# Kernel optimization log

Hardware: AMD Instinct MI355X
Metric: run time of the kernel (lower is better)

## Reference

```python
import jax, jax.numpy as jnp
import numpy as np

N, E, F_IN, H, C, G, OUT = 50000, 800000, 128, 4, 64, 64, 16
NEG_SLOPE = 0.2


def _gat_layer(x, src, dst, W, a_src, a_dst, b):
    # x: [N, Fin]; W: [Fin, H*C]; a_src/a_dst: [H, C]; b: [H*C]
    h = (x @ W).reshape(N, H, C)                      # [N,H,C]
    e_src = jnp.einsum('nhc,hc->nh', h, a_src)        # [N,H]
    e_dst = jnp.einsum('nhc,hc->nh', h, a_dst)
    e = jax.nn.leaky_relu(e_src[src] + e_dst[dst], NEG_SLOPE)  # [Etot,H]
    # segment softmax over edges sharing a destination node
    m = jax.ops.segment_max(e, dst, num_segments=N)   # [N,H]
    ex = jnp.exp(e - m[dst])
    s = jax.ops.segment_sum(ex, dst, num_segments=N)  # [N,H]
    alpha = ex / s[dst]                               # [Etot,H]
    msg = h[src] * alpha[:, :, None]                  # [Etot,H,C]
    out = jax.ops.segment_sum(msg, dst, num_segments=N)
    return out.reshape(N, H * C) + b


def setup_inputs() -> dict:
    key = jax.random.key(0)
    ks = jax.random.split(key, 12)
    x = jax.random.normal(ks[0], (N, F_IN), dtype=jnp.float32)
    edge_index = jax.random.randint(ks[1], (2, E), 0, N, dtype=jnp.int64)
    batch = jnp.sort(jax.random.randint(ks[2], (N,), 0, G, dtype=jnp.int64))
    hc = H * C
    W1 = jax.random.normal(ks[3], (F_IN, hc), dtype=jnp.float32) / np.sqrt(F_IN)
    a_src1 = jax.random.normal(ks[4], (H, C), dtype=jnp.float32) / np.sqrt(C)
    a_dst1 = jax.random.normal(ks[5], (H, C), dtype=jnp.float32) / np.sqrt(C)
    b1 = jnp.zeros((hc,), dtype=jnp.float32)
    W2 = jax.random.normal(ks[6], (hc, hc), dtype=jnp.float32) / np.sqrt(hc)
    a_src2 = jax.random.normal(ks[7], (H, C), dtype=jnp.float32) / np.sqrt(C)
    a_dst2 = jax.random.normal(ks[8], (H, C), dtype=jnp.float32) / np.sqrt(C)
    b2 = jnp.zeros((hc,), dtype=jnp.float32)
    Wlin = jax.random.normal(ks[9], (hc, OUT), dtype=jnp.float32) / np.sqrt(hc)
    blin = jnp.zeros((OUT,), dtype=jnp.float32)
    return dict(x=x, edge_index=edge_index, batch=batch,
                W1=W1, a_src1=a_src1, a_dst1=a_dst1, b1=b1,
                W2=W2, a_src2=a_src2, a_dst2=a_dst2, b2=b2,
                Wlin=Wlin, blin=blin)


def reference(x, edge_index, batch, W1, a_src1, a_dst1, b1,
              W2, a_src2, a_dst2, b2, Wlin, blin):
    # add self-loops (PyG GATConv default add_self_loops=True)
    loops = jnp.arange(N, dtype=edge_index.dtype)
    src = jnp.concatenate([edge_index[0], loops])
    dst = jnp.concatenate([edge_index[1], loops])
    h = jax.nn.relu(_gat_layer(x, src, dst, W1, a_src1, a_dst1, b1))
    h = jax.nn.relu(_gat_layer(h, src, dst, W2, a_src2, a_dst2, b2))
    # global mean pool over graphs
    sums = jax.ops.segment_sum(h, batch, num_segments=G)          # [G, H*C]
    cnt = jax.ops.segment_sum(jnp.ones((N,), h.dtype), batch, num_segments=G)
    pooled = sums / jnp.maximum(cnt, 1.0)[:, None]
    return pooled @ Wlin + blin                                    # [G, OUT]
```

## Files before the change

kernel.cpp:

```cpp
#include <hip/hip_runtime.h>
#include <hip/hip_fp16.h>

#define NN   50000
#define EE   800000
#define ETOT 850000
#define FIN  128
#define HC   256
#define NH   4
#define CH   64
#define NG   64
#define NOUT 16
#define NEG_SLOPE 0.2f

#define NBUCK 391
#define BCAP  4096
#define EPB   4096
#define NEB   208

typedef _Float16 f16x8 __attribute__((ext_vector_type(8)));
typedef float    f32x4 __attribute__((ext_vector_type(4)));

__global__ __launch_bounds__(256) void edge_bucket(const int* __restrict__ ei,
                                                   int* __restrict__ bucket_counts,
                                                   unsigned* __restrict__ buckets) {
    __shared__ int h[NBUCK];
    __shared__ int bb[NBUCK];
    const int tid = threadIdx.x;
    const int e0  = blockIdx.x * EPB;

    for (int t = tid; t < NBUCK; t += 256) h[t] = 0;
    __syncthreads();

    int srcs[16], dsts[16];
#pragma unroll
    for (int k = 0; k < 16; ++k) {
        int i = e0 + k * 256 + tid;
        int s = 0, d = -1;
        if (i < ETOT) {
            s = (i < EE) ? ei[i] : (i - EE);
            d = (i < EE) ? ei[EE + i] : (i - EE);
            atomicAdd(&h[d >> 7], 1);
        }
        srcs[k] = s; dsts[k] = d;
    }
    __syncthreads();

    for (int t = tid; t < NBUCK; t += 256) {
        bb[t] = atomicAdd(&bucket_counts[t], h[t]);
        h[t]  = 0;
    }
    __syncthreads();

#pragma unroll
    for (int k = 0; k < 16; ++k) {
        int d = dsts[k];
        if (d >= 0) {
            int b = d >> 7;
            int r = atomicAdd(&h[b], 1);
            int idx = bb[b] + r;
            if (idx < BCAP)
                buckets[(size_t)b * BCAP + idx] =
                    (unsigned)srcs[k] | ((unsigned)(d & 127) << 16);
        }
    }
}

__global__ __launch_bounds__(512) void bucket_scan(const int* __restrict__ counts,
                                                   int* __restrict__ basep,
                                                   int* __restrict__ rowptr) {
    __shared__ int lds[512];
    const int tid = threadIdx.x;
    int v = (tid < NBUCK) ? counts[tid] : 0;
    lds[tid] = v;
    __syncthreads();
    for (int off = 1; off < 512; off <<= 1) {
        int t = (tid >= off) ? lds[tid - off] : 0;
        __syncthreads();
        lds[tid] += t;
        __syncthreads();
    }
    if (tid < NBUCK) basep[tid] = lds[tid] - v;
    if (tid == 0) rowptr[NN] = ETOT;
}

__global__ __launch_bounds__(256) void bucket_to_csr(const unsigned* __restrict__ buckets,
                                                     const int* __restrict__ bucket_counts,
                                                     const int* __restrict__ bucket_base,
                                                     int* __restrict__ rowptr,
                                                     int* __restrict__ csr) {
    __shared__ int h[128], c[128], sc[128];
    const int b = blockIdx.x, tid = threadIdx.x;
    const int nb   = bucket_counts[b];
    const int base = bucket_base[b];

    if (tid < 128) h[tid] = 0;
    __syncthreads();
    for (int i = tid; i < nb; i += 256) {
        unsigned p = buckets[(size_t)b * BCAP + i];
        atomicAdd(&h[p >> 16], 1);
    }
    __syncthreads();
    if (tid < 128) sc[tid] = h[tid];
    __syncthreads();
    for (int off = 1; off < 128; off <<= 1) {
        int t = (tid < 128 && tid >= off) ? sc[tid - off] : 0;
        __syncthreads();
        if (tid < 128) sc[tid] += t;
        __syncthreads();
    }
    if (tid < 128) {
        int excl = sc[tid] - h[tid];
        c[tid] = excl;
        int node = (b << 7) + tid;
        if (node < NN) rowptr[node] = base + excl;
    }
    __syncthreads();
    for (int i = tid; i < nb; i += 256) {
        unsigned p = buckets[(size_t)b * BCAP + i];
        int pos = atomicAdd(&c[p >> 16], 1);
        csr[base + pos] = (int)(p & 0xFFFFu);
    }
}

__global__ void f32_to_f16_vec(const float* __restrict__ in, __half* __restrict__ out,
                               int n4) {
    int i = blockIdx.x * 256 + threadIdx.x;
    if (i >= n4) return;
    float4 v = *(const float4*)&in[(size_t)i * 4];
    __half h[4] = {__float2half(v.x), __float2half(v.y), __float2half(v.z), __float2half(v.w)};
    *(uint2*)&out[(size_t)i * 4] = *(uint2*)h;
}

__global__ void w_transpose_f16(const float* __restrict__ W, __half* __restrict__ Wt,
                                int K) {
    int idx = blockIdx.x * 256 + threadIdx.x;
    if (idx >= K * HC) return;
    int n = idx / K, k = idx - n * K;
    Wt[idx] = __float2half(W[(size_t)k * HC + n]);
}

__global__ __launch_bounds__(256) void gemm_f16(const __half* __restrict__ A16,
                                                const __half* __restrict__ Bt16,
                                                __half* __restrict__ C16,
                                                const float* __restrict__ a_src,
                                                const float* __restrict__ a_dst,
                                                float* __restrict__ es,
                                                float* __restrict__ ed,
                                                int M, int K) {
    __shared__ char lds[32768];
    const int tid  = threadIdx.x;
    const int m0   = blockIdx.y * 128;
    const int n0   = blockIdx.x * 128;
    const int wid  = tid >> 6, lane = tid & 63;
    const int wr   = wid >> 1, wc = wid & 1;
    const int l15  = lane & 15, l4 = lane >> 4;
    const int trow = tid >> 3;
    const int tcol = (tid & 7) * 8;

    f32x4 acc[4][4] = {};

    for (int k0 = 0; k0 < K; k0 += 64) {
        __syncthreads();
#pragma unroll
        for (int it = 0; it < 4; ++it) {
            int row = trow + it * 32;
            uint4 v = make_uint4(0u, 0u, 0u, 0u);
            int gr = m0 + row;
            if (gr < M) v = *(const uint4*)&A16[(size_t)gr * K + k0 + tcol];
            int off = (row * 128 + tcol * 2) ^ ((row & 7) << 4);
            *(uint4*)(lds + off) = v;
            uint4 w = *(const uint4*)&Bt16[(size_t)(n0 + row) * K + k0 + tcol];
            int offb = 16384 + ((row * 128 + tcol * 2) ^ ((row & 7) << 4));
            *(uint4*)(lds + offb) = w;
        }
        __syncthreads();
#pragma unroll
        for (int ks = 0; ks < 2; ++ks) {
            f16x8 af[4], bf[4];
#pragma unroll
            for (int i = 0; i < 4; ++i) {
                int rowA = wr * 64 + i * 16 + l15;
                int offA = (rowA * 128 + ks * 64 + l4 * 16) ^ ((rowA & 7) << 4);
                af[i] = *(const f16x8*)(lds + offA);
                int rowB = wc * 64 + i * 16 + l15;
                int offB = 16384 + ((rowB * 128 + ks * 64 + l4 * 16) ^ ((rowB & 7) << 4));
                bf[i] = *(const f16x8*)(lds + offB);
            }
#pragma unroll
            for (int i = 0; i < 4; ++i)
#pragma unroll
                for (int j = 0; j < 4; ++j)
                    acc[i][j] = __builtin_amdgcn_mfma_f32_16x16x32_f16(af[i], bf[j], acc[i][j], 0, 0, 0);
        }
    }
#pragma unroll
    for (int i = 0; i < 4; ++i) {
#pragma unroll
        for (int r = 0; r < 4; ++r) {
            int row = m0 + wr * 64 + i * 16 + l4 * 4 + r;
            if (row < M) {
#pragma unroll
                for (int j = 0; j < 4; ++j) {
                    int col = n0 + wc * 64 + j * 16 + l15;
                    C16[(size_t)row * HC + col] = __float2half(acc[i][j][r]);
                }
            }
        }
    }
    const int hd = blockIdx.x * 2 + wc;
    float as_[4], ad_[4];
#pragma unroll
    for (int j = 0; j < 4; ++j) {
        int c = j * 16 + l15;
        as_[j] = a_src[hd * CH + c];
        ad_[j] = a_dst[hd * CH + c];
    }
#pragma unroll
    for (int i = 0; i < 4; ++i) {
#pragma unroll
        for (int r = 0; r < 4; ++r) {
            float ps = 0.f, pd = 0.f;
#pragma unroll
            for (int j = 0; j < 4; ++j) {
                ps = fmaf(acc[i][j][r], as_[j], ps);
                pd = fmaf(acc[i][j][r], ad_[j], pd);
            }
#pragma unroll
            for (int mm = 8; mm; mm >>= 1) {
                ps += __shfl_xor(ps, mm);
                pd += __shfl_xor(pd, mm);
            }
            int row = m0 + wr * 64 + i * 16 + l4 * 4 + r;
            if (l15 == 0 && row < M) {
                es[row * NH + hd] = ps;
                ed[row * NH + hd] = pd;
            }
        }
    }
}

__global__ __launch_bounds__(256) void gat_fused(const __half* __restrict__ hfeat,
                                                 const float* __restrict__ es,
                                                 const float* __restrict__ ed,
                                                 const int* __restrict__ rowptr,
                                                 const int* __restrict__ csr_src,
                                                 const float* __restrict__ bias,
                                                 __half* __restrict__ out16) {
    const int node = blockIdx.x * 4 + (threadIdx.x >> 6);
    const int lane = threadIdx.x & 63;
    if (node >= NN) return;
    const int start = rowptr[node];
    const int deg   = rowptr[node + 1] - start;

    const int hh = lane & 3;
    const int el = lane >> 2;
    float4 ed4 = *(const float4*)&ed[node * NH];
    float ednh = (hh & 1) ? ((hh & 2) ? ed4.w : ed4.y)
                          : ((hh & 2) ? ed4.z : ed4.x);

    float mx = -1e30f;
    for (int j = el; j < deg; j += 16) {
        int src = csr_src[start + j];
        float e = es[src * NH + hh] + ednh;
        e = (e > 0.f) ? e : NEG_SLOPE * e;
        mx = fmaxf(mx, e);
    }
#pragma unroll
    for (int off = 4; off < 64; off <<= 1) mx = fmaxf(mx, __shfl_xor(mx, off));

    float sm = 0.f;
    for (int j = el; j < deg; j += 16) {
        int src = csr_src[start + j];
        float e = es[src * NH + hh] + ednh;
        e = (e > 0.f) ? e : NEG_SLOPE * e;
        sm += __expf(e - mx);
    }
#pragma unroll
    for (int off = 4; off < 64; off <<= 1) sm += __shfl_xor(sm, off);

    const int sub = lane >> 5;
    const int cl  = lane & 31;
    const int hsel = cl >> 3;
    const float mh  = __shfl(mx, hsel);
    const float ish = 1.0f / __shfl(sm, hsel);
    const float ehn = __shfl(ednh, hsel);

    float acc[8] = {0.f, 0.f, 0.f, 0.f, 0.f, 0.f, 0.f, 0.f};
    int j = 0;
    for (; j + 3 < deg; j += 4) {
        int jj0 = start + j + sub;
        int jj1 = start + j + 2 + sub;
        int s0 = csr_src[jj0];
        int s1 = csr_src[jj1];
        float e0 = es[s0 * NH + hsel] + ehn;
        float e1 = es[s1 * NH + hsel] + ehn;
        e0 = (e0 > 0.f) ? e0 : NEG_SLOPE * e0;
        e1 = (e1 > 0.f) ? e1 : NEG_SLOPE * e1;
        float a0 = __expf(e0 - mh) * ish;
        float a1 = __expf(e1 - mh) * ish;
        uint4 r0 = *(const uint4*)&hfeat[(size_t)s0 * HC + cl * 8];
        uint4 r1 = *(const uint4*)&hfeat[(size_t)s1 * HC + cl * 8];
        const unsigned* w0 = &r0.x;
        const unsigned* w1 = &r1.x;
#pragma unroll
        for (int q = 0; q < 4; ++q) {
            float2 f0 = __half22float2(*reinterpret_cast<const __half2*>(&w0[q]));
            float2 f1 = __half22float2(*reinterpret_cast<const __half2*>(&w1[q]));
            acc[q * 2]     = fmaf(a0, f0.x, acc[q * 2]);
            acc[q * 2 + 1] = fmaf(a0, f0.y, acc[q * 2 + 1]);
            acc[q * 2]     = fmaf(a1, f1.x, acc[q * 2]);
            acc[q * 2 + 1] = fmaf(a1, f1.y, acc[q * 2 + 1]);
        }
    }
    for (; j < deg; j += 2) {
        int jj = j + sub;
        if (jj < deg) {
            int s0 = csr_src[start + jj];
            float e0 = es[s0 * NH + hsel] + ehn;
            e0 = (e0 > 0.f) ? e0 : NEG_SLOPE * e0;
            float a0 = __expf(e0 - mh) * ish;
            uint4 r0 = *(const uint4*)&hfeat[(size_t)s0 * HC + cl * 8];
            const unsigned* w0 = &r0.x;
#pragma unroll
            for (int q = 0; q < 4; ++q) {
                float2 f0 = __half22float2(*reinterpret_cast<const __half2*>(&w0[q]));
                acc[q * 2]     = fmaf(a0, f0.x, acc[q * 2]);
                acc[q * 2 + 1] = fmaf(a0, f0.y, acc[q * 2 + 1]);
            }
        }
    }
#pragma unroll
    for (int q = 0; q < 8; ++q) acc[q] += __shfl_xor(acc[q], 32);

    if (lane < 32) {
        float4 b0 = *(const float4*)&bias[cl * 8];
        float4 b1 = *(const float4*)&bias[cl * 8 + 4];
        const float* bp0 = &b0.x;
        const float* bp1 = &b1.x;
        __half h[8];
#pragma unroll
        for (int q = 0; q < 4; ++q) h[q]     = __float2half(fmaxf(acc[q]     + bp0[q], 0.f));
#pragma unroll
        for (int q = 0; q < 4; ++q) h[4 + q] = __float2half(fmaxf(acc[4 + q] + bp1[q], 0.f));
        *(uint4*)&out16[(size_t)node * HC + cl * 8] = *(uint4*)h;
    }
}

__global__ __launch_bounds__(256) void pool_sum(const __half* __restrict__ h,
                                                const int* __restrict__ batch,
                                                float* __restrict__ sums) {
    int t  = threadIdx.x;
    int n0 = blockIdx.x * 128;
    if (n0 >= NN) return;
    int cur = batch[n0];
    float acc = 0.f;
    int nend = min(n0 + 128, NN);
    for (int n = n0; n < nend; ++n) {
        int g = batch[n];
        if (g != cur) {
            atomicAdd(&sums[cur * HC + t], acc);
            acc = 0.f; cur = g;
        }
        acc += __half2float(h[(size_t)n * HC + t]);
    }
    atomicAdd(&sums[cur * HC + t], acc);
}

__global__ void batch_bounds(const int* __restrict__ batch,
                             int* __restrict__ beg, int* __restrict__ end) {
    int i = blockIdx.x * 256 + threadIdx.x;
    if (i >= NN) return;
    int g = batch[i];
    if (i == 0      || batch[i - 1] != g) beg[g] = i;
    if (i == NN - 1 || batch[i + 1] != g) end[g] = i + 1;
}

__global__ __launch_bounds__(256) void final_linear(const float* __restrict__ sums,
                                                    const int* __restrict__ beg,
                                                    const int* __restrict__ end,
                                                    const float* __restrict__ Wlin,
                                                    const float* __restrict__ blin,
                                                    float* __restrict__ out) {
    int idx = blockIdx.x * 256 + threadIdx.x;
    if (idx >= NG * NOUT) return;
    int g = idx >> 4, o = idx & 15;
    float cnt = (float)(end[g] - beg[g]);
    float invc = 1.f / fmaxf(cnt, 1.f);
    float acc = 0.f;
    for (int k = 0; k < HC; ++k) acc += sums[g * HC + k] * Wlin[k * NOUT + o];
    out[idx] = acc * invc + blin[o];
}

extern "C" void kernel_launch(void* const* d_in, const int* in_sizes, int n_in,
                              void* d_out, int out_size, void* d_ws, size_t ws_size,
                              hipStream_t stream) {
    const float* x      = (const float*)d_in[0];
    const int*   ei     = (const int*)d_in[1];
    const int*   batch  = (const int*)d_in[2];
    const float* W1     = (const float*)d_in[3];
    const float* a_src1 = (const float*)d_in[4];
    const float* a_dst1 = (const float*)d_in[5];
    const float* b1     = (const float*)d_in[6];
    const float* W2     = (const float*)d_in[7];
    const float* a_src2 = (const float*)d_in[8];
    const float* a_dst2 = (const float*)d_in[9];
    const float* b2     = (const float*)d_in[10];
    const float* Wlin   = (const float*)d_in[11];
    const float* blin   = (const float*)d_in[12];
    float* out = (float*)d_out;

    char* p = (char*)d_ws;
    auto take = [&](size_t bytes) {
        char* r = p;
        p += (bytes + 255) & ~(size_t)255;
        return r;
    };
    __half*   bufT16 = (__half*)take((size_t)NN * HC * 2);
    __half*   bufH16 = (__half*)take((size_t)NN * HC * 2);
    __half*   x16    = (__half*)take((size_t)NN * FIN * 2);
    __half*   w1t    = (__half*)take((size_t)FIN * HC * 2);
    __half*   w2t    = (__half*)take((size_t)HC * HC * 2);
    float*    es     = (float*)take((size_t)NN * NH * 4);
    float*    ed     = (float*)take((size_t)NN * NH * 4);
    int*      rowptr = (int*)take((size_t)(NN + 1) * 4);
    int*      csr    = (int*)take((size_t)ETOT * 4);
    unsigned* buckets= (unsigned*)take((size_t)NBUCK * BCAP * 4);
    int*      bcnt   = (int*)take((size_t)NBUCK * 4);
    int*      bbase  = (int*)take((size_t)NBUCK * 4);
    float*    sums   = (float*)take((size_t)NG * HC * 4);
    int*      gbeg   = (int*)take((size_t)NG * 4);
    int*      gend   = (int*)take((size_t)NG * 4);

    hipMemsetAsync(bcnt, 0, (size_t)NBUCK * 4, stream);
    hipMemsetAsync(sums, 0, (size_t)NG * HC * 4, stream);
    hipMemsetAsync(gbeg, 0, (size_t)NG * 4, stream);
    hipMemsetAsync(gend, 0, (size_t)NG * 4, stream);

    edge_bucket<<<NEB, 256, 0, stream>>>(ei, bcnt, buckets);
    bucket_scan<<<1, 512, 0, stream>>>(bcnt, bbase, rowptr);
    bucket_to_csr<<<NBUCK, 256, 0, stream>>>(buckets, bcnt, bbase, rowptr, csr);
    f32_to_f16_vec<<<(NN * FIN / 4 + 255) / 256, 256, 0, stream>>>(x, x16, NN * FIN / 4);
    w_transpose_f16<<<(FIN * HC + 255) / 256, 256, 0, stream>>>(W1, w1t, FIN);
    w_transpose_f16<<<(HC * HC + 255) / 256, 256, 0, stream>>>(W2, w2t, HC);

    gemm_f16<<<dim3(2, (NN + 127) / 128), 256, 0, stream>>>(x16, w1t, bufT16,
                                                            a_src1, a_dst1, es, ed, NN, FIN);
    gat_fused<<<(NN + 3) / 4, 256, 0, stream>>>(bufT16, es, ed, rowptr, csr, b1, bufH16);

    gemm_f16<<<dim3(2, (NN + 127) / 128), 256, 0, stream>>>(bufH16, w2t, bufT16,
                                                            a_src2, a_dst2, es, ed, NN, HC);
    gat_fused<<<(NN + 3) / 4, 256, 0, stream>>>(bufT16, es, ed, rowptr, csr, b2, bufH16);

    pool_sum<<<(NN + 127) / 128, 256, 0, stream>>>(bufH16, batch, sums);
    batch_bounds<<<(NN + 255) / 256, 256, 0, stream>>>(batch, gbeg, gend);
    final_linear<<<4, 256, 0, stream>>>(sums, gbeg, gend, Wlin, blin, out);
}
```

Measured before the change: 296.9 us.

## Split GAT aggregation into softmax-alpha pass and channel-sliced gather

Replaces the fused per-node softmax+gather kernel with two kernels. The first computes normalized attention weights per edge and head and stores them as fp16 head planes. The second launches 8 blocks per node group, each handling a 32-channel slice and gathering 8-byte pieces of source features. The aim is to improve L2 locality of the random feature gathers, since each channel slice of hfeat is a smaller working set, and to spread the work over more parallel blocks. In exchange it adds an extra kernel launch per layer, writes and reads an alpha buffer, reads csr eight times per node, and issues smaller, less efficient loads.

```diff
diff --git a/kernel.cpp b/kernel.cpp
--- a/kernel.cpp
+++ b/kernel.cpp
@@ -239,13 +239,11 @@
     }
 }
 
-__global__ __launch_bounds__(256) void gat_fused(const __half* __restrict__ hfeat,
-                                                 const float* __restrict__ es,
-                                                 const float* __restrict__ ed,
-                                                 const int* __restrict__ rowptr,
-                                                 const int* __restrict__ csr_src,
-                                                 const float* __restrict__ bias,
-                                                 __half* __restrict__ out16) {
+__global__ __launch_bounds__(256) void softmax_alpha_planes(const float* __restrict__ es,
+                                                            const float* __restrict__ ed,
+                                                            const int* __restrict__ rowptr,
+                                                            const int* __restrict__ csr,
+                                                            __half* __restrict__ alphap) {
     const int node = blockIdx.x * 4 + (threadIdx.x >> 6);
     const int lane = threadIdx.x & 63;
     if (node >= NN) return;
@@ -260,7 +258,7 @@
 
     float mx = -1e30f;
     for (int j = el; j < deg; j += 16) {
-        int src = csr_src[start + j];
+        int src = csr[start + j];
         float e = es[src * NH + hh] + ednh;
         e = (e > 0.f) ? e : NEG_SLOPE * e;
         mx = fmaxf(mx, e);
@@ -270,79 +268,70 @@
 
     float sm = 0.f;
     for (int j = el; j < deg; j += 16) {
-        int src = csr_src[start + j];
+        int src = csr[start + j];
         float e = es[src * NH + hh] + ednh;
         e = (e > 0.f) ? e : NEG_SLOPE * e;
         sm += __expf(e - mx);
     }
 #pragma unroll
     for (int off = 4; off < 64; off <<= 1) sm += __shfl_xor(sm, off);
-
-    const int sub = lane >> 5;
-    const int cl  = lane & 31;
-    const int hsel = cl >> 3;
-    const float mh  = __shfl(mx, hsel);
-    const float ish = 1.0f / __shfl(sm, hsel);
-    const float ehn = __shfl(ednh, hsel);
-
-    float acc[8] = {0.f, 0.f, 0.f, 0.f, 0.f, 0.f, 0.f, 0.f};
-    int j = 0;
-    for (; j + 3 < deg; j += 4) {
-        int jj0 = start + j + sub;
-        int jj1 = start + j + 2 + sub;
-        int s0 = csr_src[jj0];
-        int s1 = csr_src[jj1];
-        float e0 = es[s0 * NH + hsel] + ehn;
-        float e1 = es[s1 * NH + hsel] + ehn;
-        e0 = (e0 > 0.f) ? e0 : NEG_SLOPE * e0;
-        e1 = (e1 > 0.f) ? e1 : NEG_SLOPE * e1;
-        float a0 = __expf(e0 - mh) * ish;
-        float a1 = __expf(e1 - mh) * ish;
-        uint4 r0 = *(const uint4*)&hfeat[(size_t)s0 * HC + cl * 8];
-        uint4 r1 = *(const uint4*)&hfeat[(size_t)s1 * HC + cl * 8];
-        const unsigned* w0 = &r0.x;
-        const unsigned* w1 = &r1.x;
-#pragma unroll
-        for (int q = 0; q < 4; ++q) {
-            float2 f0 = __half22float2(*reinterpret_cast<const __half2*>(&w0[q]));
-            float2 f1 = __half22float2(*reinterpret_cast<const __half2*>(&w1[q]));
-            acc[q * 2]     = fmaf(a0, f0.x, acc[q * 2]);
-            acc[q * 2 + 1] = fmaf(a0, f0.y, acc[q * 2 + 1]);
-            acc[q * 2]     = fmaf(a1, f1.x, acc[q * 2]);
-            acc[q * 2 + 1] = fmaf(a1, f1.y, acc[q * 2 + 1]);
-        }
-    }
-    for (; j < deg; j += 2) {
-        int jj = j + sub;
-        if (jj < deg) {
-            int s0 = csr_src[start + jj];
-            float e0 = es[s0 * NH + hsel] + ehn;
-            e0 = (e0 > 0.f) ? e0 : NEG_SLOPE * e0;
-            float a0 = __expf(e0 - mh) * ish;
-            uint4 r0 = *(const uint4*)&hfeat[(size_t)s0 * HC + cl * 8];
-            const unsigned* w0 = &r0.x;
-#pragma unroll
-            for (int q = 0; q < 4; ++q) {
-                float2 f0 = __half22float2(*reinterpret_cast<const __half2*>(&w0[q]));
-                acc[q * 2]     = fmaf(a0, f0.x, acc[q * 2]);
-                acc[q * 2 + 1] = fmaf(a0, f0.y, acc[q * 2 + 1]);
-            }
-        }
-    }
-#pragma unroll
-    for (int q = 0; q < 8; ++q) acc[q] += __shfl_xor(acc[q], 32);
-
-    if (lane < 32) {
-        float4 b0 = *(const float4*)&bias[cl * 8];
-        float4 b1 = *(const float4*)&bias[cl * 8 + 4];
-        const float* bp0 = &b0.x;
-        const float* bp1 = &b1.x;
-        __half h[8];
-#pragma unroll
-        for (int q = 0; q < 4; ++q) h[q]     = __float2half(fmaxf(acc[q]     + bp0[q], 0.f));
-#pragma unroll
-        for (int q = 0; q < 4; ++q) h[4 + q] = __float2half(fmaxf(acc[4 + q] + bp1[q], 0.f));
-        *(uint4*)&out16[(size_t)node * HC + cl * 8] = *(uint4*)h;
+    const float inv = 1.0f / sm;
+
+    for (int j = el; j < deg; j += 16) {
+        int src = csr[start + j];
+        float e = es[src * NH + hh] + ednh;
+        e = (e > 0.f) ? e : NEG_SLOPE * e;
+        alphap[(size_t)hh * ETOT + start + j] = __float2half(__expf(e - mx) * inv);
+    }
+}
+
+__global__ __launch_bounds__(256) void gat_gather_sliced(const __half* __restrict__ hfeat,
+                                                         const __half* __restrict__ alphap,
+                                                         const int* __restrict__ rowptr,
+                                                         const int* __restrict__ csr,
+                                                         const float* __restrict__ bias,
+                                                         __half* __restrict__ out16) {
+    const int c    = blockIdx.x & 7;
+    const int ng   = blockIdx.x >> 3;
+    const int node = ng * 4 + (threadIdx.x >> 6);
+    const int lane = threadIdx.x & 63;
+    if (node >= NN) return;
+    const int g      = lane >> 3;
+    const int cl     = lane & 7;
+    const int hs     = c >> 1;
+    const int chbase = c * 32 + cl * 4;
+    const int start  = rowptr[node];
+    const int deg    = rowptr[node + 1] - start;
+    const __half* ap = alphap + (size_t)hs * ETOT;
+
+    float a0 = 0.f, a1 = 0.f, a2 = 0.f, a3 = 0.f;
+    for (int j = g; j < deg; j += 8) {
+        int e   = start + j;
+        int src = csr[e];
+        float a = __half2float(ap[e]);
+        uint2 r = *(const uint2*)&hfeat[(size_t)src * HC + chbase];
+        float2 f0 = __half22float2(*reinterpret_cast<const __half2*>(&r.x));
+        float2 f1 = __half22float2(*reinterpret_cast<const __half2*>(&r.y));
+        a0 = fmaf(a, f0.x, a0);
+        a1 = fmaf(a, f0.y, a1);
+        a2 = fmaf(a, f1.x, a2);
+        a3 = fmaf(a, f1.y, a3);
+    }
+#pragma unroll
+    for (int off = 8; off < 64; off <<= 1) {
+        a0 += __shfl_xor(a0, off);
+        a1 += __shfl_xor(a1, off);
+        a2 += __shfl_xor(a2, off);
+        a3 += __shfl_xor(a3, off);
+    }
+    if (lane < 8) {
+        float4 b = *(const float4*)&bias[chbase];
+        __half h[4];
+        h[0] = __float2half(fmaxf(a0 + b.x, 0.f));
+        h[1] = __float2half(fmaxf(a1 + b.y, 0.f));
+        h[2] = __float2half(fmaxf(a2 + b.z, 0.f));
+        h[3] = __float2half(fmaxf(a3 + b.w, 0.f));
+        *(uint2*)&out16[(size_t)node * HC + chbase] = *(uint2*)h;
     }
 }
 
@@ -427,6 +416,7 @@
     unsigned* buckets= (unsigned*)take((size_t)NBUCK * BCAP * 4);
     int*      bcnt   = (int*)take((size_t)NBUCK * 4);
     int*      bbase  = (int*)take((size_t)NBUCK * 4);
+    __half*   alphap = (__half*)take((size_t)NH * ETOT * 2);
     float*    sums   = (float*)take((size_t)NG * HC * 4);
     int*      gbeg   = (int*)take((size_t)NG * 4);
     int*      gend   = (int*)take((size_t)NG * 4);
@@ -443,13 +433,17 @@
     w_transpose_f16<<<(FIN * HC + 255) / 256, 256, 0, stream>>>(W1, w1t, FIN);
     w_transpose_f16<<<(HC * HC + 255) / 256, 256, 0, stream>>>(W2, w2t, HC);
 
+    const int ngrp = (NN + 3) / 4;
+
     gemm_f16<<<dim3(2, (NN + 127) / 128), 256, 0, stream>>>(x16, w1t, bufT16,
                                                             a_src1, a_dst1, es, ed, NN, FIN);
-    gat_fused<<<(NN + 3) / 4, 256, 0, stream>>>(bufT16, es, ed, rowptr, csr, b1, bufH16);
+    softmax_alpha_planes<<<ngrp, 256, 0, stream>>>(es, ed, rowptr, csr, alphap);
+    gat_gather_sliced<<<ngrp * 8, 256, 0, stream>>>(bufT16, alphap, rowptr, csr, b1, bufH16);
 
     gemm_f16<<<dim3(2, (NN + 127) / 128), 256, 0, stream>>>(bufH16, w2t, bufT16,
                                                             a_src2, a_dst2, es, ed, NN, HC);
-    gat_fused<<<(NN + 3) / 4, 256, 0, stream>>>(bufT16, es, ed, rowptr, csr, b2, bufH16);
+    softmax_alpha_planes<<<ngrp, 256, 0, stream>>>(es, ed, rowptr, csr, alphap);
+    gat_gather_sliced<<<ngrp * 8, 256, 0, stream>>>(bufT16, alphap, rowptr, csr, b2, bufH16);
 
     pool_sum<<<(NN + 127) / 128, 256, 0, stream>>>(bufH16, batch, sums);
     batch_bounds<<<(NN + 255) / 256, 256, 0, stream>>>(batch, gbeg, gend);
```

Result: slower. 511.9 us (+72.4%).
